# Optimization experiments

Hardware: AMD Instinct MI355X
Metric: run time of the kernel (lower is better)

## Reference

```python
import jax, jax.numpy as jnp
import numpy as np

N = 4
TMAX = 20
EPS = 1e-06
POST_MULT = 2.0


def setup_inputs() -> dict:
    key = jax.random.key(0)
    ks = jax.random.split(key, 8)
    T, C = 8192, 1024
    return {
        "x": jax.random.normal(ks[0], (T, N, C), dtype=jnp.float32),
        "f_out": jax.random.normal(ks[1], (T, C), dtype=jnp.float32),
        "mix": jax.random.normal(ks[2], (T, 2 * N + N * N), dtype=jnp.float32),
        "invr": jax.random.uniform(ks[3], (T,), dtype=jnp.float32),
        "alpha_pre": jax.random.uniform(ks[4], (1,), dtype=jnp.float32),
        "alpha_post": jax.random.uniform(ks[5], (1,), dtype=jnp.float32),
        "alpha_res": jax.random.uniform(ks[6], (1,), dtype=jnp.float32),
        "bias": jax.random.normal(ks[7], (2 * N + N * N,), dtype=jnp.float32),
    }


def _sinkhorn(r):
    # r: (T, N, N) logits. Row-softmax exp, then TMAX row/col normalizations.
    r = jnp.exp(r - jnp.max(r, axis=-1, keepdims=True))
    def body(_, r):
        r = r / (jnp.sum(r, axis=-1, keepdims=True) + EPS)  # row normalize
        r = r / (jnp.sum(r, axis=-2, keepdims=True) + EPS)  # col normalize
        return r
    return jax.lax.fori_loop(0, TMAX, body, r)


def reference(x, f_out, mix, invr, alpha_pre, alpha_post, alpha_res, bias):
    T = mix.shape[0]
    s = mix * invr[:, None]  # (T, 24)
    h_pre = jax.nn.sigmoid(s[:, :N] * alpha_pre + bias[:N])                      # (T, N)
    h_post = jax.nn.sigmoid(s[:, N:2 * N] * alpha_post + bias[N:2 * N]) * POST_MULT  # (T, N)
    r = (s[:, 2 * N:] * alpha_res + bias[2 * N:]).reshape(T, N, N)
    h_res = _sinkhorn(r)  # (T, N, N), doubly-normalized mixing matrix
    # pre-aggregate the N residual streams into one (input to the wrapped sublayer)
    y_pre = jnp.einsum("tn,tnc->tc", h_pre, x)
    # residual remix + gated sublayer output broadcast back to N streams
    out = jnp.einsum("tji,tic->tjc", h_res, x) + h_post[:, :, None] * f_out[:, None, :]
    return y_pre, out
```

## Files before the change

kernel.cpp:

```cpp
#include <hip/hip_runtime.h>
#include <math.h>

#define NN 4
#define TMAX 20
#define EPS 1e-6f
#define POST_MULT 2.0f

typedef float vfloat4 __attribute__((ext_vector_type(4)));

__global__ __launch_bounds__(256) void fused_kernel(
    const float* __restrict__ x,
    const float* __restrict__ f_out,
    const float* __restrict__ mix,
    const float* __restrict__ invr,
    const float* __restrict__ alpha_pre,
    const float* __restrict__ alpha_post,
    const float* __restrict__ alpha_res,
    const float* __restrict__ bias,
    float* __restrict__ y_pre,
    float* __restrict__ out,
    int C)
{
    __shared__ float sm[24];

    const int t   = blockIdx.x;
    const int tid = threadIdx.x;

    if (tid < 16) {
        const int lane = tid;
        const float ir = invr[t];

        float r = mix[t * 24 + 8 + lane] * ir * alpha_res[0] + bias[8 + lane];
        float m = r;
        m = fmaxf(m, __shfl_xor(m, 1));
        m = fmaxf(m, __shfl_xor(m, 2));
        r = __expf(r - m);
        #pragma unroll
        for (int it = 0; it < TMAX; ++it) {
            float rs = r;
            rs += __shfl_xor(rs, 1);
            rs += __shfl_xor(rs, 2);
            r = r / (rs + EPS);
            float cs = r;
            cs += __shfl_xor(cs, 4);
            cs += __shfl_xor(cs, 8);
            r = r / (cs + EPS);
        }
        sm[8 + lane] = r;

        if (lane < 8) {
            const float a = (lane < NN) ? alpha_pre[0] : alpha_post[0];
            const float z = mix[t * 24 + lane] * ir * a + bias[lane];
            float sg = 1.0f / (1.0f + __expf(-z));
            if (lane >= NN) sg *= POST_MULT;
            sm[lane] = sg;
        }
    }
    __syncthreads();

    const float hp0 = sm[0], hp1 = sm[1], hp2 = sm[2], hp3 = sm[3];
    const float hq0 = sm[4], hq1 = sm[5], hq2 = sm[6], hq3 = sm[7];
    float hr[NN][NN];
    #pragma unroll
    for (int j = 0; j < NN; ++j)
        #pragma unroll
        for (int i = 0; i < NN; ++i)
            hr[j][i] = sm[8 + j * 4 + i];

    const int NV = C >> 2;
    const vfloat4* xv4 = (const vfloat4*)(x + (size_t)t * NN * C);
    const vfloat4* fv4 = (const vfloat4*)(f_out + (size_t)t * C);
    vfloat4* yp4 = (vfloat4*)(y_pre + (size_t)t * C);
    vfloat4* o4  = (vfloat4*)(out + (size_t)t * NN * C);

    for (int v = tid; v < NV; v += blockDim.x) {
        vfloat4 xv[NN];
        #pragma unroll
        for (int n = 0; n < NN; ++n) xv[n] = xv4[n * NV + v];
        const vfloat4 fv = fv4[v];

        vfloat4 yv = hp0 * xv[0] + hp1 * xv[1] + hp2 * xv[2] + hp3 * xv[3];
        __builtin_nontemporal_store(yv, &yp4[v]);

        const float hq[NN] = {hq0, hq1, hq2, hq3};
        #pragma unroll
        for (int j = 0; j < NN; ++j) {
            vfloat4 ov = hq[j] * fv;
            #pragma unroll
            for (int i = 0; i < NN; ++i) ov += hr[j][i] * xv[i];
            __builtin_nontemporal_store(ov, &o4[j * NV + v]);
        }
    }
}

extern "C" void kernel_launch(void* const* d_in, const int* in_sizes, int n_in,
                              void* d_out, int out_size, void* d_ws, size_t ws_size,
                              hipStream_t stream) {
    const float* x          = (const float*)d_in[0];
    const float* f_out      = (const float*)d_in[1];
    const float* mix        = (const float*)d_in[2];
    const float* invr       = (const float*)d_in[3];
    const float* alpha_pre  = (const float*)d_in[4];
    const float* alpha_post = (const float*)d_in[5];
    const float* alpha_res  = (const float*)d_in[6];
    const float* bias       = (const float*)d_in[7];

    const int T = in_sizes[3];
    const int C = in_sizes[1] / T;

    float* y_pre = (float*)d_out;
    float* out   = (float*)d_out + (size_t)T * C;
    (void)d_ws; (void)ws_size;

    fused_kernel<<<T, 256, 0, stream>>>(x, f_out, mix, invr, alpha_pre,
                                        alpha_post, alpha_res, bias,
                                        y_pre, out, C);
}
```

Baseline: 303.8 us.

## Process four tokens per block with register double-buffered prefetch

Each block now handles KT=4 tokens. Sixty-four threads compute the four Sinkhorn/sigmoid coefficient sets in parallel, and the first token's x/f_out loads are issued before the barrier so they overlap the Sinkhorn compute. Inside the loop, the next token's inputs are prefetched into registers while the current one is computed and stored. This hides load latency and spreads the serial Sinkhorn cost over more work, at the cost of a quarter as many blocks and higher register pressure. With C=1024 each thread runs the v loop once, so the __syncthreads inside that loop is reached uniformly.

```diff
diff --git a/kernel.cpp b/kernel.cpp
--- a/kernel.cpp
+++ b/kernel.cpp
@@ -5,6 +5,7 @@
 #define TMAX 20
 #define EPS 1e-6f
 #define POST_MULT 2.0f
+#define KT 4
 
 typedef float vfloat4 __attribute__((ext_vector_type(4)));
 
@@ -19,76 +20,104 @@
     const float* __restrict__ bias,
     float* __restrict__ y_pre,
     float* __restrict__ out,
-    int C)
+    int C, int T)
 {
-    __shared__ float sm[24];
+    __shared__ float sm[KT][24];
 
-    const int t   = blockIdx.x;
+    const int t0  = blockIdx.x * KT;
     const int tid = threadIdx.x;
 
-    if (tid < 16) {
-        const int lane = tid;
-        const float ir = invr[t];
+    if (tid < 16 * KT) {
+        const int g    = tid >> 4;
+        const int lane = tid & 15;
+        const int t    = t0 + g;
+        if (t < T) {
+            const float ir = invr[t];
 
-        float r = mix[t * 24 + 8 + lane] * ir * alpha_res[0] + bias[8 + lane];
-        float m = r;
-        m = fmaxf(m, __shfl_xor(m, 1));
-        m = fmaxf(m, __shfl_xor(m, 2));
-        r = __expf(r - m);
-        #pragma unroll
-        for (int it = 0; it < TMAX; ++it) {
-            float rs = r;
-            rs += __shfl_xor(rs, 1);
-            rs += __shfl_xor(rs, 2);
-            r = r / (rs + EPS);
-            float cs = r;
-            cs += __shfl_xor(cs, 4);
-            cs += __shfl_xor(cs, 8);
-            r = r / (cs + EPS);
-        }
-        sm[8 + lane] = r;
+            float r = mix[t * 24 + 8 + lane] * ir * alpha_res[0] + bias[8 + lane];
+            float m = r;
+            m = fmaxf(m, __shfl_xor(m, 1));
+            m = fmaxf(m, __shfl_xor(m, 2));
+            r = __expf(r - m);
+            #pragma unroll
+            for (int it = 0; it < TMAX; ++it) {
+                float rs = r;
+                rs += __shfl_xor(rs, 1);
+                rs += __shfl_xor(rs, 2);
+                r = r / (rs + EPS);
+                float cs = r;
+                cs += __shfl_xor(cs, 4);
+                cs += __shfl_xor(cs, 8);
+                r = r / (cs + EPS);
+            }
+            sm[g][8 + lane] = r;
 
-        if (lane < 8) {
-            const float a = (lane < NN) ? alpha_pre[0] : alpha_post[0];
-            const float z = mix[t * 24 + lane] * ir * a + bias[lane];
-            float sg = 1.0f / (1.0f + __expf(-z));
-            if (lane >= NN) sg *= POST_MULT;
-            sm[lane] = sg;
+            if (lane < 8) {
+                const float a = (lane < NN) ? alpha_pre[0] : alpha_post[0];
+                const float z = mix[t * 24 + lane] * ir * a + bias[lane];
+                float sg = 1.0f / (1.0f + __expf(-z));
+                if (lane >= NN) sg *= POST_MULT;
+                sm[g][lane] = sg;
+            }
         }
     }
-    __syncthreads();
-
-    const float hp0 = sm[0], hp1 = sm[1], hp2 = sm[2], hp3 = sm[3];
-    const float hq0 = sm[4], hq1 = sm[5], hq2 = sm[6], hq3 = sm[7];
-    float hr[NN][NN];
-    #pragma unroll
-    for (int j = 0; j < NN; ++j)
-        #pragma unroll
-        for (int i = 0; i < NN; ++i)
-            hr[j][i] = sm[8 + j * 4 + i];
 
     const int NV = C >> 2;
-    const vfloat4* xv4 = (const vfloat4*)(x + (size_t)t * NN * C);
-    const vfloat4* fv4 = (const vfloat4*)(f_out + (size_t)t * C);
-    vfloat4* yp4 = (vfloat4*)(y_pre + (size_t)t * C);
-    vfloat4* o4  = (vfloat4*)(out + (size_t)t * NN * C);
 
     for (int v = tid; v < NV; v += blockDim.x) {
-        vfloat4 xv[NN];
+        vfloat4 xA[NN], fA;
+        {
+            const vfloat4* xp = (const vfloat4*)(x + (size_t)t0 * NN * C);
+            const vfloat4* fp = (const vfloat4*)(f_out + (size_t)t0 * C);
+            #pragma unroll
+            for (int n = 0; n < NN; ++n) xA[n] = xp[n * NV + v];
+            fA = fp[v];
+        }
+        __syncthreads();
+
         #pragma unroll
-        for (int n = 0; n < NN; ++n) xv[n] = xv4[n * NV + v];
-        const vfloat4 fv = fv4[v];
+        for (int k = 0; k < KT; ++k) {
+            const int t = t0 + k;
+            if (t >= T) break;
 
-        vfloat4 yv = hp0 * xv[0] + hp1 * xv[1] + hp2 * xv[2] + hp3 * xv[3];
-        __builtin_nontemporal_store(yv, &yp4[v]);
+            vfloat4 xB[NN], fB;
+            const bool have_next = (k + 1 < KT) && (t + 1 < T);
+            if (have_next) {
+                const vfloat4* xp = (const vfloat4*)(x + (size_t)(t + 1) * NN * C);
+                const vfloat4* fp = (const vfloat4*)(f_out + (size_t)(t + 1) * C);
+                #pragma unroll
+                for (int n = 0; n < NN; ++n) xB[n] = xp[n * NV + v];
+                fB = fp[v];
+            }
 
-        const float hq[NN] = {hq0, hq1, hq2, hq3};
-        #pragma unroll
-        for (int j = 0; j < NN; ++j) {
-            vfloat4 ov = hq[j] * fv;
+            const float hp0 = sm[k][0], hp1 = sm[k][1], hp2 = sm[k][2], hp3 = sm[k][3];
+            const float hq[NN] = {sm[k][4], sm[k][5], sm[k][6], sm[k][7]};
+            float hr[NN][NN];
             #pragma unroll
-            for (int i = 0; i < NN; ++i) ov += hr[j][i] * xv[i];
-            __builtin_nontemporal_store(ov, &o4[j * NV + v]);
+            for (int j = 0; j < NN; ++j)
+                #pragma unroll
+                for (int i = 0; i < NN; ++i)
+                    hr[j][i] = sm[k][8 + j * 4 + i];
+
+            vfloat4* yp4 = (vfloat4*)(y_pre + (size_t)t * C);
+            vfloat4* o4  = (vfloat4*)(out + (size_t)t * NN * C);
+
+            vfloat4 yv = hp0 * xA[0] + hp1 * xA[1] + hp2 * xA[2] + hp3 * xA[3];
+            __builtin_nontemporal_store(yv, &yp4[v]);
+
+            #pragma unroll
+            for (int j = 0; j < NN; ++j) {
+                vfloat4 ov = hq[j] * fA;
+                #pragma unroll
+                for (int i = 0; i < NN; ++i) ov += hr[j][i] * xA[i];
+                __builtin_nontemporal_store(ov, &o4[j * NV + v]);
+            }
+
+            if (have_next) {
+                #pragma unroll
+                for (int n = 0; n < NN; ++n) xA[n] = xB[n];
+                fA = fB;
+            }
         }
     }
 }
@@ -112,7 +141,8 @@
     float* out   = (float*)d_out + (size_t)T * C;
     (void)d_ws; (void)ws_size;
 
-    fused_kernel<<<T, 256, 0, stream>>>(x, f_out, mix, invr, alpha_pre,
-                                        alpha_post, alpha_res, bias,
-                                        y_pre, out, C);
+    const int grid = (T + KT - 1) / KT;
+    fused_kernel<<<grid, 256, 0, stream>>>(x, f_out, mix, invr, alpha_pre,
+                                           alpha_post, alpha_res, bias,
+                                           y_pre, out, C, T);
 }
```

New measurement: 305.7 us. About the same (+0.6%).

## Prefetch x and f_out into registers before Sinkhorn using 64-thread blocks

Applied to the files above, without the earlier changes.

Each block shrinks from 256 to 64 threads, and every thread now holds KS=4 vector chunks. All global loads of x and f_out are issued at kernel start, before the serial Sinkhorn iterations and the barrier, so memory latency overlaps the per-row mixing-matrix computation. The cost is higher register pressure from holding 20 float4 values per thread. Coverage is also hard-wired to C <= 4*64*4, so larger C would leave columns unprocessed.

```diff
diff --git a/kernel.cpp b/kernel.cpp
--- a/kernel.cpp
+++ b/kernel.cpp
@@ -5,10 +5,11 @@
 #define TMAX 20
 #define EPS 1e-6f
 #define POST_MULT 2.0f
+#define KS 4
 
 typedef float vfloat4 __attribute__((ext_vector_type(4)));
 
-__global__ __launch_bounds__(256) void fused_kernel(
+__global__ __launch_bounds__(64) void fused_kernel(
     const float* __restrict__ x,
     const float* __restrict__ f_out,
     const float* __restrict__ mix,
@@ -25,6 +26,22 @@
 
     const int t   = blockIdx.x;
     const int tid = threadIdx.x;
+    const int NV  = C >> 2;
+
+    const vfloat4* xv4 = (const vfloat4*)(x + (size_t)t * NN * C);
+    const vfloat4* fv4 = (const vfloat4*)(f_out + (size_t)t * C);
+
+    vfloat4 xv[KS][NN];
+    vfloat4 fv[KS];
+    #pragma unroll
+    for (int k = 0; k < KS; ++k) {
+        const int v = tid + (k << 6);
+        if (v < NV) {
+            #pragma unroll
+            for (int n = 0; n < NN; ++n) xv[k][n] = xv4[n * NV + v];
+            fv[k] = fv4[v];
+        }
+    }
 
     if (tid < 16) {
         const int lane = tid;
@@ -59,7 +76,7 @@
     __syncthreads();
 
     const float hp0 = sm[0], hp1 = sm[1], hp2 = sm[2], hp3 = sm[3];
-    const float hq0 = sm[4], hq1 = sm[5], hq2 = sm[6], hq3 = sm[7];
+    const float hq[NN] = {sm[4], sm[5], sm[6], sm[7]};
     float hr[NN][NN];
     #pragma unroll
     for (int j = 0; j < NN; ++j)
@@ -67,28 +84,24 @@
         for (int i = 0; i < NN; ++i)
             hr[j][i] = sm[8 + j * 4 + i];
 
-    const int NV = C >> 2;
-    const vfloat4* xv4 = (const vfloat4*)(x + (size_t)t * NN * C);
-    const vfloat4* fv4 = (const vfloat4*)(f_out + (size_t)t * C);
     vfloat4* yp4 = (vfloat4*)(y_pre + (size_t)t * C);
     vfloat4* o4  = (vfloat4*)(out + (size_t)t * NN * C);
 
-    for (int v = tid; v < NV; v += blockDim.x) {
-        vfloat4 xv[NN];
-        #pragma unroll
-        for (int n = 0; n < NN; ++n) xv[n] = xv4[n * NV + v];
-        const vfloat4 fv = fv4[v];
+    #pragma unroll
+    for (int k = 0; k < KS; ++k) {
+        const int v = tid + (k << 6);
+        if (v < NV) {
+            vfloat4 yv = hp0 * xv[k][0] + hp1 * xv[k][1]
+                       + hp2 * xv[k][2] + hp3 * xv[k][3];
+            __builtin_nontemporal_store(yv, &yp4[v]);
 
-        vfloat4 yv = hp0 * xv[0] + hp1 * xv[1] + hp2 * xv[2] + hp3 * xv[3];
-        __builtin_nontemporal_store(yv, &yp4[v]);
-
-        const float hq[NN] = {hq0, hq1, hq2, hq3};
-        #pragma unroll
-        for (int j = 0; j < NN; ++j) {
-            vfloat4 ov = hq[j] * fv;
             #pragma unroll
-            for (int i = 0; i < NN; ++i) ov += hr[j][i] * xv[i];
-            __builtin_nontemporal_store(ov, &o4[j * NV + v]);
+            for (int j = 0; j < NN; ++j) {
+                vfloat4 ov = hq[j] * fv[k];
+                #pragma unroll
+                for (int i = 0; i < NN; ++i) ov += hr[j][i] * xv[k][i];
+                __builtin_nontemporal_store(ov, &o4[j * NV + v]);
+            }
         }
     }
 }
@@ -112,7 +125,7 @@
     float* out   = (float*)d_out + (size_t)T * C;
     (void)d_ws; (void)ws_size;
 
-    fused_kernel<<<T, 256, 0, stream>>>(x, f_out, mix, invr, alpha_pre,
-                                        alpha_post, alpha_res, bias,
-                                        y_pre, out, C);
+    fused_kernel<<<T, 64, 0, stream>>>(x, f_out, mix, invr, alpha_pre,
+                                       alpha_post, alpha_res, bias,
+                                       y_pre, out, C);
 }
```

Measured after the change: 305.0 us. Within noise of the previous version (+0.4%).
